# Kernel optimization log

Hardware: AMD Instinct MI355X
Metric: run time of the kernel (lower is better)

Reference implementation:

```python
import jax, jax.numpy as jnp
import numpy as np

B, V, C, H, W = 2, 4, 64, 256, 256
RADIUS = 2.0
R = 2  # integer splat footprint half-width = ceil(RADIUS)
EPS = 1e-8
FOCAL = 256.0


def _rt(tx, ty, tz):
    M = np.eye(4, dtype=np.float32)
    M[0, 3], M[1, 3], M[2, 3] = tx, ty, tz
    return M


def setup_inputs() -> dict:
    key = jax.random.key(0)
    k1, k2 = jax.random.split(key)
    feats = jax.random.normal(k1, (B, V, C, H, W), dtype=jnp.float32)
    # depths in [1, 5): positive, realistic metric range
    depths = 1.0 + 4.0 * jax.random.uniform(k2, (B, V, 1, H, W), dtype=jnp.float32)
    Km = np.eye(4, dtype=np.float32)
    Km[0, 0] = FOCAL; Km[1, 1] = FOCAL
    Km[0, 2] = W / 2.0; Km[1, 2] = H / 2.0
    K = jnp.asarray(np.tile(Km[None], (B, 1, 1)))
    src = np.stack([_rt(0.05 * v, 0.0, 0.0) for v in range(V)], 0)  # (V,4,4)
    src_RTs = jnp.asarray(np.tile(src[None], (B, 1, 1, 1)))
    src_RTinvs = jnp.linalg.inv(src_RTs)
    dst = _rt(0.02, 0.0, 0.1)
    dst_RTs = jnp.asarray(np.tile(dst[None, None], (B, 1, 1, 1)))
    dst_RTinvs = jnp.linalg.inv(dst_RTs)
    return {"feats": feats, "depths": depths, "K": K, "src_RTs": src_RTs,
            "src_RTinvs": src_RTinvs, "dst_RTs": dst_RTs, "dst_RTinvs": dst_RTinvs}


def _project_and_splat(feats, depths, K, src_RTinvs, dst_RTs):
    Bn, Vn, Cn, Hn, Wn = feats.shape
    N = Hn * Wn
    BV = Bn * Vn
    # pixel grid (homogeneous image coords), row-major so flat idx = y*W + x
    xs = jnp.arange(Wn, dtype=feats.dtype)
    ys = jnp.arange(Hn, dtype=feats.dtype)
    gx, gy = jnp.meshgrid(xs, ys, indexing="xy")  # (H,W)
    gx = gx.reshape(-1); gy = gy.reshape(-1)      # (N,)
    d = depths.reshape(Bn, Vn, 1, N)
    ones = jnp.ones_like(d)
    # view_to_world_coord: [x*d, y*d, d, 1] -> K^-1 -> RTinv
    proj = jnp.concatenate([gx * d, gy * d, d, ones], axis=2)  # (B,V,4,N)
    Kinv = jnp.linalg.inv(K)
    cam = jnp.einsum("bij,bvjn->bvin", Kinv, proj)
    world = jnp.einsum("bvij,bvjn->bvin", src_RTinvs, cam)
    # world_to_view: dst RT -> K -> perspective divide
    cam2 = jnp.einsum("bij,bvjn->bvin", dst_RTs.reshape(Bn, 4, 4), world)
    xyp = jnp.einsum("bij,bvjn->bvin", K, cam2)
    z = xyp[:, :, 2].reshape(BV, N)
    x = (xyp[:, :, 0] / (xyp[:, :, 2] + EPS)).reshape(BV, N)
    y = (xyp[:, :, 1] / (xyp[:, :, 2] + EPS)).reshape(BV, N)
    # radius splatting: scatter-accumulate over a (2R+1)^2 footprint,
    # linear falloff in pixel distance, soft z-buffer via 1/z weighting
    fN = feats.reshape(BV, Cn, N).transpose(0, 2, 1)  # (BV,N,C)
    acc = jnp.zeros((BV * N, Cn), feats.dtype)
    wz = jnp.zeros((BV * N, 2), feats.dtype)  # [:,0]=sum w, [:,1]=sum w*z
    boff = (jnp.arange(BV) * N)[:, None]
    px0 = jnp.round(x); py0 = jnp.round(y)
    invz = 1.0 / (z + EPS)
    for dy in range(-R, R + 1):
        for dx in range(-R, R + 1):
            px = px0 + dx; py = py0 + dy
            dist = jnp.sqrt((px - x) ** 2 + (py - y) ** 2 + EPS)
            w = jnp.maximum(0.0, 1.0 - dist / RADIUS)
            valid = (px >= 0) & (px < Wn) & (py >= 0) & (py < Hn) & (z > EPS)
            w = jnp.where(valid, w * invz, 0.0)
            ix = jnp.clip(px.astype(jnp.int32), 0, Wn - 1)
            iy = jnp.clip(py.astype(jnp.int32), 0, Hn - 1)
            idx = (boff + iy * Wn + ix).reshape(-1)
            acc = acc.at[idx].add((w[..., None] * fN).reshape(-1, Cn))
            wz = wz.at[idx].add(jnp.stack([w, w * z], -1).reshape(-1, 2))
    wsum = wz[:, 0:1]; zsum = wz[:, 1:2]
    prj_feats = (acc / (wsum + EPS)).reshape(Bn, Vn, Hn, Wn, Cn).transpose(0, 1, 4, 2, 3)
    prj_depth = (zsum / (wsum + EPS)).reshape(Bn, Vn, Hn, Wn, 1).transpose(0, 1, 4, 2, 3)
    return jnp.concatenate([prj_feats, prj_depth], axis=2)  # (B,V,C+1,H,W)


def reference(feats, depths, K, src_RTs, src_RTinvs, dst_RTs, dst_RTinvs):
    return _project_and_splat(feats, depths, K, src_RTinvs, dst_RTs)
```

## Files before the change

### kernel.cpp

```cpp
#include <hip/hip_runtime.h>

#define Wd 256
#define Hd 256
#define Nn 65536
#define Cc 64
#define Vv 4
#define Bb 2
#define BVn 8
#define EPSf 1e-8f

#define OFF_COUNT   ((size_t)0)
#define OFF_OFFS    ((size_t)2  << 20)
#define OFF_CURS    ((size_t)4  << 20)
#define OFF_ROWSUM  ((size_t)6  << 20)
#define OFF_ROWBASE (((size_t)6 << 20) + 65536)
#define OFF_STAGE1  ((size_t)8  << 20)
#define OFF_BINNED  ((size_t)16 << 20)
#define OFF_FT      ((size_t)24 << 20)
#define FT_BYTES    ((size_t)BVn * Nn * Cc * 4)
#define NEED_FULL   (OFF_FT + FT_BYTES)
#define NEED_MID    OFF_FT

__device__ inline void mat4_mul(const float* A, const float* B, float* C) {
#pragma unroll
  for (int i = 0; i < 4; i++)
#pragma unroll
    for (int j = 0; j < 4; j++) {
      float s = 0.f;
#pragma unroll
      for (int k = 0; k < 4; k++) s += A[i * 4 + k] * B[k * 4 + j];
      C[i * 4 + j] = s;
    }
}

__device__ inline void mat4_inv(const float* m, float* invOut) {
  float inv[16];
  inv[0] = m[5]*m[10]*m[15] - m[5]*m[11]*m[14] - m[9]*m[6]*m[15] +
           m[9]*m[7]*m[14] + m[13]*m[6]*m[11] - m[13]*m[7]*m[10];
  inv[4] = -m[4]*m[10]*m[15] + m[4]*m[11]*m[14] + m[8]*m[6]*m[15] -
           m[8]*m[7]*m[14] - m[12]*m[6]*m[11] + m[12]*m[7]*m[10];
  inv[8] = m[4]*m[9]*m[15] - m[4]*m[11]*m[13] - m[8]*m[5]*m[15] +
           m[8]*m[7]*m[13] + m[12]*m[5]*m[11] - m[12]*m[7]*m[9];
  inv[12] = -m[4]*m[9]*m[14] + m[4]*m[10]*m[13] + m[8]*m[5]*m[14] -
            m[8]*m[6]*m[13] - m[12]*m[5]*m[10] + m[12]*m[6]*m[9];
  inv[1] = -m[1]*m[10]*m[15] + m[1]*m[11]*m[14] + m[9]*m[2]*m[15] -
           m[9]*m[3]*m[14] - m[13]*m[2]*m[11] + m[13]*m[3]*m[10];
  inv[5] = m[0]*m[10]*m[15] - m[0]*m[11]*m[14] - m[8]*m[2]*m[15] +
           m[8]*m[3]*m[14] + m[12]*m[2]*m[11] - m[12]*m[3]*m[10];
  inv[9] = -m[0]*m[9]*m[15] + m[0]*m[11]*m[13] + m[8]*m[1]*m[15] -
           m[8]*m[3]*m[13] - m[12]*m[1]*m[11] + m[12]*m[3]*m[9];
  inv[13] = m[0]*m[9]*m[14] - m[0]*m[10]*m[13] - m[8]*m[1]*m[14] +
            m[8]*m[2]*m[13] + m[12]*m[1]*m[10] - m[12]*m[2]*m[9];
  inv[2] = m[1]*m[6]*m[15] - m[1]*m[7]*m[14] - m[5]*m[2]*m[15] +
           m[5]*m[3]*m[14] + m[13]*m[2]*m[7] - m[13]*m[3]*m[6];
  inv[6] = -m[0]*m[6]*m[15] + m[0]*m[7]*m[14] + m[4]*m[2]*m[15] -
           m[4]*m[3]*m[14] - m[12]*m[2]*m[7] + m[12]*m[3]*m[6];
  inv[10] = m[0]*m[5]*m[15] - m[0]*m[7]*m[13] - m[4]*m[1]*m[15] +
            m[4]*m[3]*m[13] + m[12]*m[1]*m[7] - m[12]*m[3]*m[5];
  inv[14] = -m[0]*m[5]*m[14] + m[0]*m[6]*m[13] + m[4]*m[1]*m[14] -
            m[4]*m[2]*m[13] - m[12]*m[1]*m[6] + m[12]*m[2]*m[5];
  inv[3] = -m[1]*m[6]*m[11] + m[1]*m[7]*m[10] + m[5]*m[2]*m[11] -
           m[5]*m[3]*m[10] - m[9]*m[2]*m[7] + m[9]*m[3]*m[6];
  inv[7] = m[0]*m[6]*m[11] - m[0]*m[7]*m[10] - m[4]*m[2]*m[11] +
           m[4]*m[3]*m[10] + m[8]*m[2]*m[7] - m[8]*m[3]*m[6];
  inv[11] = -m[0]*m[5]*m[11] + m[0]*m[7]*m[9] + m[4]*m[1]*m[11] -
            m[4]*m[3]*m[9] - m[8]*m[1]*m[7] + m[8]*m[3]*m[5];
  inv[15] = m[0]*m[5]*m[10] - m[0]*m[6]*m[9] - m[4]*m[1]*m[10] +
            m[4]*m[2]*m[9] + m[8]*m[1]*m[6] - m[8]*m[2]*m[5];
  float det = m[0]*inv[0] + m[1]*inv[4] + m[2]*inv[8] + m[3]*inv[12];
  det = 1.0f / det;
#pragma unroll
  for (int i = 0; i < 16; i++) invOut[i] = inv[i] * det;
}

__device__ inline void compute_T(const float* Kmat, const float* srcinv,
                                 const float* dstRT, int b, int bv, float* T) {
  float Kinv[16], M1[16], M2[16];
  mat4_inv(Kmat + b * 16, Kinv);
  mat4_mul(srcinv + bv * 16, Kinv, M1);
  mat4_mul(dstRT + b * 16, M1, M2);
  mat4_mul(Kmat + b * 16, M2, T);
}

__global__ __launch_bounds__(256) void transpose_kernel(
    const float* __restrict__ feats, float* __restrict__ featsT) {
  __shared__ float lds[Cc][65];
  const int bv = blockIdx.x >> 10;
  const int n0 = (blockIdx.x & 1023) << 6;
  const int t = threadIdx.x;

  const float* src = feats + (size_t)bv * Cc * Nn;
  {
    const int c_l = t >> 6;
    const int n_l = t & 63;
#pragma unroll
    for (int i = 0; i < 16; i++) {
      const int c = c_l * 16 + i;
      lds[c][n_l] = src[(size_t)c * Nn + n0 + n_l];
    }
  }
  __syncthreads();
  {
    const int c_l = t & 63;
    const int n_b = t >> 6;
    float* dst = featsT + ((size_t)bv * Nn + n0) * Cc;
#pragma unroll
    for (int i = 0; i < 16; i++) {
      const int n = n_b * 16 + i;
      dst[(size_t)n * Cc + c_l] = lds[c_l][n];
    }
  }
}

__global__ __launch_bounds__(256) void project_count_kernel(
    const float* __restrict__ depths, const float* __restrict__ Kmat,
    const float* __restrict__ srcinv, const float* __restrict__ dstRT,
    unsigned int* __restrict__ counts, float4* __restrict__ stage1) {
  const int bv = blockIdx.x >> 8;
  const int n = ((blockIdx.x & 255) << 8) | threadIdx.x;
  const int b = bv >> 2;

  __shared__ float T[16];
  if (threadIdx.x == 0) compute_T(Kmat, srcinv, dstRT, b, bv, T);
  __syncthreads();

  const float d = depths[(size_t)bv * Nn + n];
  const float gx = (float)(n & (Wd - 1));
  const float gy = (float)(n >> 8);

  const float p0 = (T[0] * gx + T[1] * gy + T[2]) * d + T[3];
  const float p1 = (T[4] * gx + T[5] * gy + T[6]) * d + T[7];
  const float z  = (T[8] * gx + T[9] * gy + T[10]) * d + T[11];

  const float ze = z + EPSf;
  const float x = p0 / ze;
  const float y = p1 / ze;
  const float px0 = rintf(x);
  const float py0 = rintf(y);

  int bin = -1;
  if (z > EPSf && px0 >= -2.0f && px0 <= (float)(Wd + 1) &&
      py0 >= -2.0f && py0 <= (float)(Hd + 1)) {
    const int bx = min(max((int)px0, 0), Wd - 1);
    const int by = min(max((int)py0, 0), Hd - 1);
    bin = (bv << 16) | (by << 8) | bx;
    atomicAdd(&counts[bin], 1u);
  }
  float4 rec;
  rec.x = x; rec.y = y; rec.z = z; rec.w = __int_as_float(bin);
  stage1[(size_t)bv * Nn + n] = rec;
}

__global__ __launch_bounds__(256) void row_sum_kernel(
    const unsigned int* __restrict__ counts, unsigned int* __restrict__ rowsum) {
  const int r = blockIdx.x * 256 + threadIdx.x;
  unsigned int s = 0;
  const unsigned int* c = counts + (size_t)r * 256;
  for (int i = 0; i < 256; i++) s += c[i];
  rowsum[r] = s;
}

__global__ __launch_bounds__(256) void scan_rows_kernel(
    const unsigned int* __restrict__ rowsum, unsigned int* __restrict__ rowbase) {
  __shared__ unsigned int part[256];
  const int t = threadIdx.x;
  unsigned int loc[8];
  unsigned int run = 0;
#pragma unroll
  for (int i = 0; i < 8; i++) {
    loc[i] = run;
    run += rowsum[t * 8 + i];
  }
  part[t] = run;
  __syncthreads();
  for (int off = 1; off < 256; off <<= 1) {
    unsigned int x = part[t];
    unsigned int y = (t >= off) ? part[t - off] : 0u;
    __syncthreads();
    part[t] = x + y;
    __syncthreads();
  }
  const unsigned int base = (t == 0) ? 0u : part[t - 1];
#pragma unroll
  for (int i = 0; i < 8; i++) rowbase[t * 8 + i] = base + loc[i];
}

__global__ __launch_bounds__(256) void bin_offsets_kernel(
    const unsigned int* __restrict__ counts, const unsigned int* __restrict__ rowbase,
    unsigned int* __restrict__ offs, unsigned int* __restrict__ curs) {
  const int r = blockIdx.x * 256 + threadIdx.x;
  unsigned int run = rowbase[r];
  const size_t base = (size_t)r * 256;
  for (int i = 0; i < 256; i++) {
    const unsigned int c = counts[base + i];
    offs[base + i] = run;
    curs[base + i] = run;
    run += c;
  }
}

__global__ __launch_bounds__(256) void fill_kernel(
    const float4* __restrict__ stage1, unsigned int* __restrict__ curs,
    float4* __restrict__ binned) {
  const int g = blockIdx.x * 256 + threadIdx.x;
  float4 rec = stage1[g];
  const int bin = __float_as_int(rec.w);
  if (bin >= 0) {
    const unsigned int slot = atomicAdd(&curs[bin], 1u);
    rec.w = __int_as_float(g & (Nn - 1));
    binned[slot] = rec;
  }
}

template <bool TRANS>
__global__ __launch_bounds__(256) void gather_kernel(
    const float* __restrict__ featsAny,
    const unsigned int* __restrict__ offs, const unsigned int* __restrict__ curs,
    const float4* __restrict__ binned, float* __restrict__ out) {
  const int bv = blockIdx.x >> 8;
  const int vrow = blockIdx.x & 255;
  const int u = threadIdx.x;

  float acc[Cc];
#pragma unroll
  for (int c = 0; c < Cc; c++) acc[c] = 0.f;
  float wsum = 0.f, wz = 0.f;

  const float uf = (float)u, vf = (float)vrow;
  const int by_lo = max(0, vrow - 2), by_hi = min(Hd - 1, vrow + 2);
  const int bx_lo = max(0, u - 2), bx_hi = min(Wd - 1, u + 2);

  for (int by = by_lo; by <= by_hi; by++) {
    const int rowb = (bv << 16) | (by << 8);
    const unsigned int s = offs[rowb + bx_lo];
    const unsigned int e = curs[rowb + bx_hi];
    for (unsigned int r = s; r < e; r++) {
      const float4 rec = binned[r];
      const float ddx = uf - rec.x;
      const float ddy = vf - rec.y;
      const float dist = sqrtf(ddx * ddx + ddy * ddy + EPSf);
      float w = 1.0f - dist * 0.5f;
      if (w > 0.f) {
        w *= 1.0f / (rec.z + EPSf);
        wsum += w;
        wz += w * rec.z;
        const int n = __float_as_int(rec.w);
        if (TRANS) {
          const float4* fs = reinterpret_cast<const float4*>(
              featsAny + ((size_t)(bv << 16 | n)) * Cc);
#pragma unroll
          for (int i = 0; i < 16; i++) {
            const float4 fv = fs[i];
            acc[4 * i + 0] += w * fv.x;
            acc[4 * i + 1] += w * fv.y;
            acc[4 * i + 2] += w * fv.z;
            acc[4 * i + 3] += w * fv.w;
          }
        } else {
          const float* fp = featsAny + ((size_t)bv * Cc << 16) + n;
#pragma unroll
          for (int c = 0; c < Cc; c++) acc[c] += w * fp[(size_t)c << 16];
        }
      }
    }
  }

  const float inv = 1.0f / (wsum + EPSf);
  const int dest = (vrow << 8) | u;
  float* ob = out + (((size_t)bv * 65) << 16) + dest;
#pragma unroll
  for (int c = 0; c < Cc; c++) ob[(size_t)c << 16] = acc[c] * inv;
  ob[(size_t)Cc << 16] = wz * inv;
}

__global__ __launch_bounds__(256) void splat_kernel(
    const float* __restrict__ feats, const float* __restrict__ depths,
    const float* __restrict__ Kmat, const float* __restrict__ srcinv,
    const float* __restrict__ dstRT, float* __restrict__ out,
    float* __restrict__ wsum) {
  const int bv = blockIdx.x >> 8;
  const int n = ((blockIdx.x & 255) << 8) | threadIdx.x;
  const int b = bv >> 2;

  __shared__ float T[16];
  if (threadIdx.x == 0) compute_T(Kmat, srcinv, dstRT, b, bv, T);
  __syncthreads();

  const float d = depths[(size_t)bv * Nn + n];
  const float gx = (float)(n & (Wd - 1));
  const float gy = (float)(n >> 8);
  const float p0 = (T[0] * gx + T[1] * gy + T[2]) * d + T[3];
  const float p1 = (T[4] * gx + T[5] * gy + T[6]) * d + T[7];
  const float z  = (T[8] * gx + T[9] * gy + T[10]) * d + T[11];
  const float ze = z + EPSf;
  const float x = p0 / ze, y = p1 / ze;
  const float zi = 1.0f / ze;
  const float px0 = rintf(x), py0 = rintf(y);
  const bool zok = (z > EPSf);

  float f[Cc];
  const float* fp = feats + (size_t)bv * Cc * Nn + n;
#pragma unroll
  for (int c = 0; c < Cc; c++) f[c] = fp[(size_t)c * Nn];

  float* outbv = out + (size_t)bv * 65 * Nn;
  float* wbv = wsum + (size_t)bv * Nn;
#pragma unroll
  for (int dy = -2; dy <= 2; dy++) {
#pragma unroll
    for (int dx = -2; dx <= 2; dx++) {
      const float px = px0 + (float)dx;
      const float py = py0 + (float)dy;
      const float ddx = px - x, ddy = py - y;
      const float dist = sqrtf(ddx * ddx + ddy * ddy + EPSf);
      float w = fmaxf(0.0f, 1.0f - dist * 0.5f);
      const bool valid = zok && (px >= 0.0f) && (px < (float)Wd) &&
                         (py >= 0.0f) && (py < (float)Hd);
      w = valid ? w * zi : 0.0f;
      if (w > 0.0f) {
        const int idx = (int)py * Wd + (int)px;
        atomicAdd(wbv + idx, w);
        atomicAdd(outbv + (size_t)Cc * Nn + idx, w * z);
#pragma unroll
        for (int c = 0; c < Cc; c++)
          atomicAdd(outbv + (size_t)c * Nn + idx, w * f[c]);
      }
    }
  }
}

__global__ __launch_bounds__(256) void norm_kernel(float* __restrict__ out,
                                                   const float* __restrict__ wsum) {
  const int t = blockIdx.x * 256 + threadIdx.x;
  const int n = t & 0xFFFF;
  const int bvc = t >> 16;
  const int bv = bvc / 65;
  const float wv = wsum[(size_t)bv * Nn + n];
  out[t] = out[t] / (wv + EPSf);
}

extern "C" void kernel_launch(void* const* d_in, const int* in_sizes, int n_in,
                              void* d_out, int out_size, void* d_ws, size_t ws_size,
                              hipStream_t stream) {
  const float* feats  = (const float*)d_in[0];
  const float* depths = (const float*)d_in[1];
  const float* Kmat   = (const float*)d_in[2];
  const float* srcinv = (const float*)d_in[4];
  const float* dstRT  = (const float*)d_in[5];
  float* out = (float*)d_out;
  char* ws = (char*)d_ws;

  if (ws_size >= NEED_MID) {
    unsigned int* counts = (unsigned int*)(ws + OFF_COUNT);
    unsigned int* offs   = (unsigned int*)(ws + OFF_OFFS);
    unsigned int* curs   = (unsigned int*)(ws + OFF_CURS);
    unsigned int* rowsum = (unsigned int*)(ws + OFF_ROWSUM);
    unsigned int* rowbase= (unsigned int*)(ws + OFF_ROWBASE);
    float4* stage1 = (float4*)(ws + OFF_STAGE1);
    float4* binned = (float4*)(ws + OFF_BINNED);
    float* featsT  = (float*)(ws + OFF_FT);

    hipMemsetAsync(counts, 0, (size_t)BVn * Nn * sizeof(unsigned int), stream);

    const bool trans = (ws_size >= NEED_FULL);
    if (trans)
      transpose_kernel<<<dim3(BVn * (Nn / 64)), dim3(256), 0, stream>>>(feats, featsT);

    project_count_kernel<<<dim3(BVn * (Nn / 256)), dim3(256), 0, stream>>>(
        depths, Kmat, srcinv, dstRT, counts, stage1);
    row_sum_kernel<<<dim3(8), dim3(256), 0, stream>>>(counts, rowsum);
    scan_rows_kernel<<<dim3(1), dim3(256), 0, stream>>>(rowsum, rowbase);
    bin_offsets_kernel<<<dim3(8), dim3(256), 0, stream>>>(counts, rowbase, offs, curs);
    fill_kernel<<<dim3(BVn * Nn / 256), dim3(256), 0, stream>>>(stage1, curs, binned);

    if (trans)
      gather_kernel<true><<<dim3(BVn * Hd), dim3(256), 0, stream>>>(
          featsT, offs, curs, binned, out);
    else
      gather_kernel<false><<<dim3(BVn * Hd), dim3(256), 0, stream>>>(
          feats, offs, curs, binned, out);
  } else {
    float* wsum = (float*)ws;
    hipMemsetAsync(out, 0, (size_t)out_size * sizeof(float), stream);
    hipMemsetAsync(wsum, 0, (size_t)BVn * Nn * sizeof(float), stream);
    splat_kernel<<<dim3(BVn * (Nn / 256)), dim3(256), 0, stream>>>(
        feats, depths, Kmat, srcinv, dstRT, out, wsum);
    norm_kernel<<<dim3(BVn * 65 * Nn / 256), dim3(256), 0, stream>>>(out, wsum);
  }
}
```

Before: 612.9 us.

## Bin features in fill and gather with one wavefront per output pixel

The separate transpose pass is removed. The fill kernel now scatters each point's 64 channels into a binned, channel-contiguous buffer next to its record. The gather kernel is remapped so one 64-lane wavefront handles one output pixel, each lane owning one channel. This replaces the 64-register per-thread accumulator and strided writes with coalesced loads. The row-sum and bin-offset kernels also switch from 8 serial-loop blocks to 2048 blocks using wave reductions and a shared-memory scan. The trade-off is that fill does strided feature reads, and every wavefront redundantly walks its neighbourhood's records.

```diff
diff --git a/kernel.cpp b/kernel.cpp
--- a/kernel.cpp
+++ b/kernel.cpp
@@ -15,11 +15,9 @@
 #define OFF_ROWSUM  ((size_t)6  << 20)
 #define OFF_ROWBASE (((size_t)6 << 20) + 65536)
 #define OFF_STAGE1  ((size_t)8  << 20)
-#define OFF_BINNED  ((size_t)16 << 20)
-#define OFF_FT      ((size_t)24 << 20)
-#define FT_BYTES    ((size_t)BVn * Nn * Cc * 4)
-#define NEED_FULL   (OFF_FT + FT_BYTES)
-#define NEED_MID    OFF_FT
+#define OFF_BREC    ((size_t)16 << 20)
+#define OFF_BFEAT   ((size_t)24 << 20)
+#define NEED_FULL   (OFF_BFEAT + ((size_t)BVn * Nn * Cc * 4))
 
 __device__ inline void mat4_mul(const float* A, const float* B, float* C) {
 #pragma unroll
@@ -82,36 +80,6 @@
   mat4_mul(Kmat + b * 16, M2, T);
 }
 
-__global__ __launch_bounds__(256) void transpose_kernel(
-    const float* __restrict__ feats, float* __restrict__ featsT) {
-  __shared__ float lds[Cc][65];
-  const int bv = blockIdx.x >> 10;
-  const int n0 = (blockIdx.x & 1023) << 6;
-  const int t = threadIdx.x;
-
-  const float* src = feats + (size_t)bv * Cc * Nn;
-  {
-    const int c_l = t >> 6;
-    const int n_l = t & 63;
-#pragma unroll
-    for (int i = 0; i < 16; i++) {
-      const int c = c_l * 16 + i;
-      lds[c][n_l] = src[(size_t)c * Nn + n0 + n_l];
-    }
-  }
-  __syncthreads();
-  {
-    const int c_l = t & 63;
-    const int n_b = t >> 6;
-    float* dst = featsT + ((size_t)bv * Nn + n0) * Cc;
-#pragma unroll
-    for (int i = 0; i < 16; i++) {
-      const int n = n_b * 16 + i;
-      dst[(size_t)n * Cc + c_l] = lds[c_l][n];
-    }
-  }
-}
-
 __global__ __launch_bounds__(256) void project_count_kernel(
     const float* __restrict__ depths, const float* __restrict__ Kmat,
     const float* __restrict__ srcinv, const float* __restrict__ dstRT,
@@ -153,11 +121,15 @@
 
 __global__ __launch_bounds__(256) void row_sum_kernel(
     const unsigned int* __restrict__ counts, unsigned int* __restrict__ rowsum) {
-  const int r = blockIdx.x * 256 + threadIdx.x;
-  unsigned int s = 0;
-  const unsigned int* c = counts + (size_t)r * 256;
-  for (int i = 0; i < 256; i++) s += c[i];
-  rowsum[r] = s;
+  const int r = blockIdx.x;
+  const int t = threadIdx.x;
+  __shared__ unsigned int sh[4];
+  unsigned int c = counts[(size_t)r * 256 + t];
+#pragma unroll
+  for (int off = 32; off >= 1; off >>= 1) c += __shfl_down(c, off, 64);
+  if ((t & 63) == 0) sh[t >> 6] = c;
+  __syncthreads();
+  if (t == 0) rowsum[r] = sh[0] + sh[1] + sh[2] + sh[3];
 }
 
 __global__ __launch_bounds__(256) void scan_rows_kernel(
@@ -188,46 +160,61 @@
 __global__ __launch_bounds__(256) void bin_offsets_kernel(
     const unsigned int* __restrict__ counts, const unsigned int* __restrict__ rowbase,
     unsigned int* __restrict__ offs, unsigned int* __restrict__ curs) {
-  const int r = blockIdx.x * 256 + threadIdx.x;
-  unsigned int run = rowbase[r];
-  const size_t base = (size_t)r * 256;
-  for (int i = 0; i < 256; i++) {
-    const unsigned int c = counts[base + i];
-    offs[base + i] = run;
-    curs[base + i] = run;
-    run += c;
-  }
+  const int r = blockIdx.x;
+  const int t = threadIdx.x;
+  __shared__ unsigned int sh[256];
+  const unsigned int c = counts[(size_t)r * 256 + t];
+  sh[t] = c;
+  __syncthreads();
+  for (int off = 1; off < 256; off <<= 1) {
+    unsigned int x = sh[t];
+    unsigned int y = (t >= off) ? sh[t - off] : 0u;
+    __syncthreads();
+    sh[t] = x + y;
+    __syncthreads();
+  }
+  const unsigned int excl = ((t == 0) ? 0u : sh[t - 1]) + rowbase[r];
+  offs[(size_t)r * 256 + t] = excl;
+  curs[(size_t)r * 256 + t] = excl;
 }
 
 __global__ __launch_bounds__(256) void fill_kernel(
-    const float4* __restrict__ stage1, unsigned int* __restrict__ curs,
-    float4* __restrict__ binned) {
+    const float4* __restrict__ stage1, const float* __restrict__ feats,
+    unsigned int* __restrict__ curs, float4* __restrict__ brec,
+    float4* __restrict__ bfeat) {
   const int g = blockIdx.x * 256 + threadIdx.x;
   float4 rec = stage1[g];
   const int bin = __float_as_int(rec.w);
-  if (bin >= 0) {
-    const unsigned int slot = atomicAdd(&curs[bin], 1u);
-    rec.w = __int_as_float(g & (Nn - 1));
-    binned[slot] = rec;
-  }
-}
-
-template <bool TRANS>
+  if (bin < 0) return;
+  const unsigned int slot = atomicAdd(&curs[bin], 1u);
+  const int n = g & (Nn - 1);
+  const int bv = g >> 16;
+  brec[slot] = rec;
+  const float* fp = feats + ((size_t)bv * Cc << 16) + n;
+  float4* dst = bfeat + ((size_t)slot << 4);
+#pragma unroll
+  for (int q = 0; q < 16; q++) {
+    float4 vv;
+    vv.x = fp[(size_t)(4 * q + 0) << 16];
+    vv.y = fp[(size_t)(4 * q + 1) << 16];
+    vv.z = fp[(size_t)(4 * q + 2) << 16];
+    vv.w = fp[(size_t)(4 * q + 3) << 16];
+    dst[q] = vv;
+  }
+}
+
 __global__ __launch_bounds__(256) void gather_kernel(
-    const float* __restrict__ featsAny,
     const unsigned int* __restrict__ offs, const unsigned int* __restrict__ curs,
-    const float4* __restrict__ binned, float* __restrict__ out) {
-  const int bv = blockIdx.x >> 8;
-  const int vrow = blockIdx.x & 255;
-  const int u = threadIdx.x;
-
-  float acc[Cc];
-#pragma unroll
-  for (int c = 0; c < Cc; c++) acc[c] = 0.f;
-  float wsum = 0.f, wz = 0.f;
-
-  const float uf = (float)u, vf = (float)vrow;
-  const int by_lo = max(0, vrow - 2), by_hi = min(Hd - 1, vrow + 2);
+    const float4* __restrict__ brec, const float* __restrict__ bfeat,
+    float* __restrict__ out) {
+  const int bv = blockIdx.x >> 14;
+  const int v = (blockIdx.x >> 6) & 255;
+  const int u = ((blockIdx.x & 63) << 2) | (threadIdx.x >> 6);
+  const int lane = threadIdx.x & 63;
+
+  float acc = 0.f, wsum = 0.f, wz = 0.f;
+  const float uf = (float)u, vf = (float)v;
+  const int by_lo = max(0, v - 2), by_hi = min(Hd - 1, v + 2);
   const int bx_lo = max(0, u - 2), bx_hi = min(Wd - 1, u + 2);
 
   for (int by = by_lo; by <= by_hi; by++) {
@@ -235,7 +222,7 @@
     const unsigned int s = offs[rowb + bx_lo];
     const unsigned int e = curs[rowb + bx_hi];
     for (unsigned int r = s; r < e; r++) {
-      const float4 rec = binned[r];
+      const float4 rec = brec[r];
       const float ddx = uf - rec.x;
       const float ddy = vf - rec.y;
       const float dist = sqrtf(ddx * ddx + ddy * ddy + EPSf);
@@ -244,33 +231,16 @@
         w *= 1.0f / (rec.z + EPSf);
         wsum += w;
         wz += w * rec.z;
-        const int n = __float_as_int(rec.w);
-        if (TRANS) {
-          const float4* fs = reinterpret_cast<const float4*>(
-              featsAny + ((size_t)(bv << 16 | n)) * Cc);
-#pragma unroll
-          for (int i = 0; i < 16; i++) {
-            const float4 fv = fs[i];
-            acc[4 * i + 0] += w * fv.x;
-            acc[4 * i + 1] += w * fv.y;
-            acc[4 * i + 2] += w * fv.z;
-            acc[4 * i + 3] += w * fv.w;
-          }
-        } else {
-          const float* fp = featsAny + ((size_t)bv * Cc << 16) + n;
-#pragma unroll
-          for (int c = 0; c < Cc; c++) acc[c] += w * fp[(size_t)c << 16];
-        }
+        acc += w * bfeat[((size_t)r << 6) + lane];
       }
     }
   }
 
   const float inv = 1.0f / (wsum + EPSf);
-  const int dest = (vrow << 8) | u;
+  const int dest = (v << 8) | u;
   float* ob = out + (((size_t)bv * 65) << 16) + dest;
-#pragma unroll
-  for (int c = 0; c < Cc; c++) ob[(size_t)c << 16] = acc[c] * inv;
-  ob[(size_t)Cc << 16] = wz * inv;
+  ob[(size_t)lane << 16] = acc * inv;
+  if (lane == 0) ob[(size_t)Cc << 16] = wz * inv;
 }
 
 __global__ __launch_bounds__(256) void splat_kernel(
@@ -281,11 +251,9 @@
   const int bv = blockIdx.x >> 8;
   const int n = ((blockIdx.x & 255) << 8) | threadIdx.x;
   const int b = bv >> 2;
-
   __shared__ float T[16];
   if (threadIdx.x == 0) compute_T(Kmat, srcinv, dstRT, b, bv, T);
   __syncthreads();
-
   const float d = depths[(size_t)bv * Nn + n];
   const float gx = (float)(n & (Wd - 1));
   const float gy = (float)(n >> 8);
@@ -297,12 +265,10 @@
   const float zi = 1.0f / ze;
   const float px0 = rintf(x), py0 = rintf(y);
   const bool zok = (z > EPSf);
-
   float f[Cc];
   const float* fp = feats + (size_t)bv * Cc * Nn + n;
 #pragma unroll
   for (int c = 0; c < Cc; c++) f[c] = fp[(size_t)c * Nn];
-
   float* outbv = out + (size_t)bv * 65 * Nn;
   float* wbv = wsum + (size_t)bv * Nn;
 #pragma unroll
@@ -350,35 +316,28 @@
   float* out = (float*)d_out;
   char* ws = (char*)d_ws;
 
-  if (ws_size >= NEED_MID) {
+  if (ws_size >= NEED_FULL) {
     unsigned int* counts = (unsigned int*)(ws + OFF_COUNT);
     unsigned int* offs   = (unsigned int*)(ws + OFF_OFFS);
     unsigned int* curs   = (unsigned int*)(ws + OFF_CURS);
     unsigned int* rowsum = (unsigned int*)(ws + OFF_ROWSUM);
     unsigned int* rowbase= (unsigned int*)(ws + OFF_ROWBASE);
     float4* stage1 = (float4*)(ws + OFF_STAGE1);
-    float4* binned = (float4*)(ws + OFF_BINNED);
-    float* featsT  = (float*)(ws + OFF_FT);
+    float4* brec   = (float4*)(ws + OFF_BREC);
+    float4* bfeat4 = (float4*)(ws + OFF_BFEAT);
+    const float* bfeat = (const float*)(ws + OFF_BFEAT);
 
     hipMemsetAsync(counts, 0, (size_t)BVn * Nn * sizeof(unsigned int), stream);
-
-    const bool trans = (ws_size >= NEED_FULL);
-    if (trans)
-      transpose_kernel<<<dim3(BVn * (Nn / 64)), dim3(256), 0, stream>>>(feats, featsT);
 
     project_count_kernel<<<dim3(BVn * (Nn / 256)), dim3(256), 0, stream>>>(
         depths, Kmat, srcinv, dstRT, counts, stage1);
-    row_sum_kernel<<<dim3(8), dim3(256), 0, stream>>>(counts, rowsum);
+    row_sum_kernel<<<dim3(2048), dim3(256), 0, stream>>>(counts, rowsum);
     scan_rows_kernel<<<dim3(1), dim3(256), 0, stream>>>(rowsum, rowbase);
-    bin_offsets_kernel<<<dim3(8), dim3(256), 0, stream>>>(counts, rowbase, offs, curs);
-    fill_kernel<<<dim3(BVn * Nn / 256), dim3(256), 0, stream>>>(stage1, curs, binned);
-
-    if (trans)
-      gather_kernel<true><<<dim3(BVn * Hd), dim3(256), 0, stream>>>(
-          featsT, offs, curs, binned, out);
-    else
-      gather_kernel<false><<<dim3(BVn * Hd), dim3(256), 0, stream>>>(
-          feats, offs, curs, binned, out);
+    bin_offsets_kernel<<<dim3(2048), dim3(256), 0, stream>>>(counts, rowbase, offs, curs);
+    fill_kernel<<<dim3(BVn * Nn / 256), dim3(256), 0, stream>>>(
+        stage1, feats, curs, brec, bfeat4);
+    gather_kernel<<<dim3(BVn * Hd * (Wd / 4)), dim3(256), 0, stream>>>(
+        offs, curs, brec, bfeat, out);
   } else {
     float* wsum = (float*)ws;
     hipMemsetAsync(out, 0, (size_t)out_size * sizeof(float), stream);
```

Measured after the change: 1.331 ms. 117% more time.
